# Kernel optimization log

Hardware: AMD Instinct MI355X
Metric: run time of the kernel (lower is better)

## Reference

```python
import jax, jax.numpy as jnp
import numpy as np

L, H = 6, 8          # n_layer, n_head
LN_EPS = 1e-5


def _ln(x, g, b):
    mu = jnp.mean(x, axis=-1, keepdims=True)
    var = jnp.mean((x - mu) ** 2, axis=-1, keepdims=True)
    return (x - mu) * jax.lax.rsqrt(var + LN_EPS) * g + b


def setup_inputs() -> dict:
    key = jax.random.key(0)
    B, T, V, D = 2, 2048, 32000, 512
    F = 4 * D
    std = 0.02
    ks = jax.random.split(key, 8)
    idx = jax.random.randint(ks[0], (B, T), 0, V)
    wte = jax.random.normal(ks[1], (V, D), dtype=jnp.float32) * std
    wpe = jax.random.normal(ks[2], (T, D), dtype=jnp.float32) * std
    qkv_w = jax.random.normal(ks[3], (L, D, 3 * D), dtype=jnp.float32) * std
    proj_w = jax.random.normal(ks[4], (L, D, D), dtype=jnp.float32) * std
    fc1_w = jax.random.normal(ks[5], (L, D, F), dtype=jnp.float32) * std
    fc2_w = jax.random.normal(ks[6], (L, F, D), dtype=jnp.float32) * std
    return dict(
        idx=idx, wte=wte, wpe=wpe,
        ln1_g=jnp.ones((L, D), jnp.float32), ln1_b=jnp.zeros((L, D), jnp.float32),
        qkv_w=qkv_w, qkv_b=jnp.zeros((L, 3 * D), jnp.float32),
        proj_w=proj_w, proj_b=jnp.zeros((L, D), jnp.float32),
        ln2_g=jnp.ones((L, D), jnp.float32), ln2_b=jnp.zeros((L, D), jnp.float32),
        fc1_w=fc1_w, fc1_b=jnp.zeros((L, F), jnp.float32),
        fc2_w=fc2_w, fc2_b=jnp.zeros((L, D), jnp.float32),
        lnf_g=jnp.ones((D,), jnp.float32), lnf_b=jnp.zeros((D,), jnp.float32),
    )


def reference(idx, wte, wpe, ln1_g, ln1_b, qkv_w, qkv_b, proj_w, proj_b,
              ln2_g, ln2_b, fc1_w, fc1_b, fc2_w, fc2_b, lnf_g, lnf_b):
    B, T = idx.shape
    D = wte.shape[1]
    hd = D // H
    scale = 1.0 / jnp.sqrt(jnp.asarray(hd, wte.dtype))
    x = wte[idx] + wpe[:T]                      # [B,T,D]
    mask = jnp.tril(jnp.ones((T, T), dtype=bool))

    def block(x, p):
        g1, b1, Wqkv, bqkv, Wp, bp, g2, b2, W1, bf1, W2, bf2 = p
        h = _ln(x, g1, b1)
        qkv = h @ Wqkv + bqkv                   # [B,T,3D]
        q, k, v = jnp.split(qkv, 3, axis=-1)
        q = q.reshape(B, T, H, hd)
        k = k.reshape(B, T, H, hd)
        v = v.reshape(B, T, H, hd)
        att = jnp.einsum('bqhd,bkhd->bhqk', q, k) * scale
        att = jnp.where(mask, att, -jnp.inf)
        att = jax.nn.softmax(att, axis=-1)
        y = jnp.einsum('bhqk,bkhd->bqhd', att, v).reshape(B, T, D)
        x = x + y @ Wp + bp
        h = _ln(x, g2, b2)
        x = x + jax.nn.gelu(h @ W1 + bf1, approximate=False) @ W2 + bf2
        return x, None

    x, _ = jax.lax.scan(block, x, (ln1_g, ln1_b, qkv_w, qkv_b, proj_w, proj_b,
                                   ln2_g, ln2_b, fc1_w, fc1_b, fc2_w, fc2_b))
    x = _ln(x, lnf_g, lnf_b)
    logits = x @ wte.T                          # tied head, [B,T,V]
    return logits
```

## Files before the change

kernel.cpp:

```cpp
#include <hip/hip_runtime.h>
#include <hip/hip_bf16.h>
#include <math.h>

#define BB 2
#define TT 2048
#define DD 512
#define HH 8
#define HD 64
#define FF 2048
#define VV 32000
#define LL 6
#define MM (BB * TT)

typedef unsigned int   u32;
typedef unsigned short u16;
typedef __attribute__((ext_vector_type(8))) short short8;
typedef __attribute__((ext_vector_type(4))) float f32x4;

__device__ __forceinline__ u16 f2bf_bits(float f)
{
    __hip_bfloat16 h = __float2bfloat16(f);
    u16 u;
    __builtin_memcpy(&u, &h, 2);
    return u;
}

__device__ __forceinline__ void gll16(const u16* g, u16* l)
{
    __builtin_amdgcn_global_load_lds(
        (const __attribute__((address_space(1))) u32*)g,
        (__attribute__((address_space(3))) u32*)l,
        16, 0, 0);
}

__device__ __forceinline__ float gelu_exact(float v)
{
    return 0.5f * v * (1.0f + erff(v * 0.70710678118654752440f));
}

__device__ __forceinline__ u16* swp(u16* base, int row, int col)
{
    int off = (row * 128 + col * 2) ^ ((row & 7) << 4);
    return (u16*)((char*)base + off);
}
__device__ __forceinline__ const u16* swpc(const u16* base, int row, int col)
{
    int off = (row * 128 + col * 2) ^ ((row & 7) << 4);
    return (const u16*)((const char*)base + off);
}

__global__ __launch_bounds__(128)
void embed_kernel(const int* __restrict__ idx, const float* __restrict__ wte,
                  const float* __restrict__ wpe, float* __restrict__ x)
{
    int row = blockIdx.x;
    int t = row & (TT - 1);
    int tok = idx[row];
    const float4* wt = (const float4*)(wte + (size_t)tok * DD);
    const float4* wp = (const float4*)(wpe + (size_t)t * DD);
    float4 a = wt[threadIdx.x];
    float4 p = wp[threadIdx.x];
    float4 r;
    r.x = a.x + p.x; r.y = a.y + p.y; r.z = a.z + p.z; r.w = a.w + p.w;
    ((float4*)(x + (size_t)row * DD))[threadIdx.x] = r;
}

__global__ __launch_bounds__(256)
void ln_kernel(const float* __restrict__ x, const float* __restrict__ g,
               const float* __restrict__ b, u16* __restrict__ out)
{
    int row = blockIdx.x;
    const float* xr = x + (size_t)row * DD;
    int tid = threadIdx.x;
    float v1 = xr[tid], v2 = xr[tid + 256];
    float s = v1 + v2;
    float ss = v1 * v1 + v2 * v2;
    #pragma unroll
    for (int o = 32; o; o >>= 1) {
        s  += __shfl_xor(s, o);
        ss += __shfl_xor(ss, o);
    }
    __shared__ float sred[4], ssred[4];
    int wid = tid >> 6, lane = tid & 63;
    if (lane == 0) { sred[wid] = s; ssred[wid] = ss; }
    __syncthreads();
    s  = sred[0] + sred[1] + sred[2] + sred[3];
    ss = ssred[0] + ssred[1] + ssred[2] + ssred[3];
    float mu  = s * (1.0f / DD);
    float var = ss * (1.0f / DD) - mu * mu;
    float rs  = rsqrtf(var + 1e-5f);
    u16* orow = out + (size_t)row * DD;
    orow[tid]       = f2bf_bits((v1 - mu) * rs * g[tid]       + b[tid]);
    orow[tid + 256] = f2bf_bits((v2 - mu) * rs * g[tid + 256] + b[tid + 256]);
}

__global__ __launch_bounds__(256)
void weight_prep_kernel(const float* __restrict__ qkv_w, const float* __restrict__ proj_w,
                        const float* __restrict__ fc1_w, const float* __restrict__ fc2_w,
                        u16* __restrict__ wqa, u16* __restrict__ wpa,
                        u16* __restrict__ w1a, u16* __restrict__ w2a)
{
    int id = blockIdx.x;
    int l = id / 3072, r = id % 3072;
    const float* in; u16* out; int K, N, tt;
    if (r < 768)       { in = qkv_w + (size_t)l * DD * 3 * DD; out = wqa + (size_t)l * 3 * DD * DD; K = DD; N = 3 * DD; tt = r; }
    else if (r < 1024) { in = proj_w + (size_t)l * DD * DD;    out = wpa + (size_t)l * DD * DD;    K = DD; N = DD;     tt = r - 768; }
    else if (r < 2048) { in = fc1_w + (size_t)l * DD * FF;     out = w1a + (size_t)l * DD * FF;    K = DD; N = FF;     tt = r - 1024; }
    else               { in = fc2_w + (size_t)l * FF * DD;     out = w2a + (size_t)l * FF * DD;    K = FF; N = DD;     tt = r - 2048; }
    int ntx = N >> 5;
    int n0 = (tt % ntx) << 5, k0 = (tt / ntx) << 5;
    __shared__ float tile[32][33];
    int tx = threadIdx.x & 31, ty = threadIdx.x >> 5;
    #pragma unroll
    for (int i = 0; i < 4; ++i)
        tile[ty + i * 8][tx] = in[(size_t)(k0 + ty + i * 8) * N + n0 + tx];
    __syncthreads();
    #pragma unroll
    for (int i = 0; i < 4; ++i)
        out[(size_t)(n0 + ty + i * 8) * K + k0 + tx] = f2bf_bits(tile[tx][ty + i * 8]);
}

__global__ __launch_bounds__(256)
void cvt_kernel(const float* __restrict__ in, u16* __restrict__ out, int n4)
{
    int i = blockIdx.x * 256 + threadIdx.x;
    if (i >= n4) return;
    float4 v = ((const float4*)in)[i];
    ushort4 o;
    o.x = f2bf_bits(v.x); o.y = f2bf_bits(v.y);
    o.z = f2bf_bits(v.z); o.w = f2bf_bits(v.w);
    ((ushort4*)out)[i] = o;
}

template<int BN, bool GELU_ACT, bool RESID, bool OUTBF16, bool QKV_SPLIT>
__global__ __launch_bounds__(256)
void mfma_gemm(const u16* __restrict__ A, const u16* __restrict__ Bt,
               const float* __restrict__ bias, const float* __restrict__ resid,
               void* __restrict__ Cout, u16* __restrict__ Vout,
               int M, int N, int K)
{
    constexpr int NJ = BN / 32;
    __shared__ u16 As[128 * 64];
    __shared__ u16 Bs[BN * 64];

    const int tid  = threadIdx.x;
    const int lane = tid & 63;
    const int w    = tid >> 6;
    const int wr   = w >> 1, wc = w & 1;

    const int nbx = gridDim.x;
    const int nwg = nbx * gridDim.y;
    int bid = blockIdx.y * nbx + blockIdx.x;
    int swz = (bid & 7) * (nwg >> 3) + (bid >> 3);
    const int m0 = (swz / nbx) * 128;
    const int n0 = (swz % nbx) * BN;

    const int trow = tid >> 3;
    const int tcol = (tid & 7) * 8;
    const u16* ga = A  + (size_t)(m0 + trow) * K + tcol;
    const u16* gb = Bt + (size_t)(n0 + trow) * K + tcol;
    u16* la = As + tid * 8;
    u16* lb = Bs + tid * 8;

    f32x4 acc[4][NJ] = {};

    const int fr = lane & 15;
    const int fk = (lane >> 4) * 8;

    for (int k0 = 0; k0 < K; k0 += 64) {
        #pragma unroll
        for (int p = 0; p < 4; ++p)
            gll16(ga + k0 + (size_t)p * 32 * K, la + p * 2048);
        #pragma unroll
        for (int p = 0; p < NJ; ++p)
            gll16(gb + k0 + (size_t)p * 32 * K, lb + p * 2048);
        asm volatile("s_waitcnt vmcnt(0)" ::: "memory");
        __syncthreads();

        #pragma unroll
        for (int ks = 0; ks < 2; ++ks) {
            short8 af[4], bfr[NJ];
            #pragma unroll
            for (int f = 0; f < 4; ++f)
                af[f]  = *(const short8*)&As[(wr * 64 + f * 16 + fr) * 64 + ks * 32 + fk];
            #pragma unroll
            for (int f = 0; f < NJ; ++f)
                bfr[f] = *(const short8*)&Bs[(wc * (BN / 2) + f * 16 + fr) * 64 + ks * 32 + fk];
            #pragma unroll
            for (int i = 0; i < 4; ++i)
                #pragma unroll
                for (int j = 0; j < NJ; ++j)
                    acc[i][j] = __builtin_amdgcn_mfma_f32_16x16x32_bf16(
                        af[i], bfr[j], acc[i][j], 0, 0, 0);
        }
        __syncthreads();
    }

    const int c0 = n0 + wc * (BN / 2) + fr;
    const int r0 = m0 + wr * 64 + ((lane >> 4) << 2);
    #pragma unroll
    for (int j = 0; j < NJ; ++j) {
        const int c = c0 + j * 16;
        const float bv = bias ? bias[c] : 0.0f;
        #pragma unroll
        for (int i = 0; i < 4; ++i) {
            #pragma unroll
            for (int r = 0; r < 4; ++r) {
                const int row = r0 + i * 16 + r;
                float v = acc[i][j][r] + bv;
                if constexpr (GELU_ACT) v = gelu_exact(v);
                if constexpr (RESID) v += resid[(size_t)row * N + c];
                if constexpr (QKV_SPLIT) {
                    if (c < 1024) {
                        ((u16*)Cout)[(size_t)row * 1024 + c] = f2bf_bits(v);
                    } else {
                        const int t = row & (TT - 1);
                        Vout[(((size_t)(row >> 11) * 512 + (c - 1024)) << 11) + t] = f2bf_bits(v);
                    }
                } else if constexpr (OUTBF16) {
                    ((u16*)Cout)[(size_t)row * N + c] = f2bf_bits(v);
                } else {
                    ((float*)Cout)[(size_t)row * N + c] = v;
                }
            }
        }
    }
}

__global__ __launch_bounds__(256)
void attn_kernel(const u16* __restrict__ qkb, const u16* __restrict__ vtb,
                 u16* __restrict__ y)
{
    const int l = blockIdx.x;
    const int u = l & 255, v = l >> 8;
    const int bh = u & 15;
    const int half = u >> 4;
    const int qt = v ? (16 + half) : (15 - half);
    const int h = bh & (HH - 1);
    const int b = bh >> 3;

    __shared__ alignas(16) u16 Qs[64 * 64];
    __shared__ alignas(16) u16 Ks[64 * 64];
    __shared__ alignas(16) u16 Vt[64 * 64];
    __shared__ alignas(16) u16 Ps[64 * 64];

    const int tid = threadIdx.x;
    const int lane = tid & 63;
    const int w = tid >> 6;
    const int ln = lane & 15, hi = lane >> 4;
    const int q0 = qt * 64;

    const u16* base  = qkb + (size_t)b * TT * 1024 + h * HD;
    const u16* vbase = vtb + (size_t)(b * 512 + h * HD) * TT;

    {
        int r = tid >> 2, c0 = (tid & 3) * 16;
        const u16* qrow = base + (size_t)(q0 + r) * 1024;
        *(short8*)swp(Qs, r, c0)     = *(const short8*)(qrow + c0);
        *(short8*)swp(Qs, r, c0 + 8) = *(const short8*)(qrow + c0 + 8);
    }

    float m[4], lsum[4];
    f32x4 oacc[4] = {};
    #pragma unroll
    for (int r = 0; r < 4; ++r) { m[r] = -INFINITY; lsum[r] = 0.0f; }

    for (int kt = 0; kt <= qt; ++kt) {
        const int k0 = kt * 64;
        __syncthreads();
        {
            int r = tid >> 2, c0 = (tid & 3) * 16;
            const u16* krow = base + (size_t)(k0 + r) * 1024 + 512;
            *(short8*)swp(Ks, r, c0)     = *(const short8*)(krow + c0);
            *(short8*)swp(Ks, r, c0 + 8) = *(const short8*)(krow + c0 + 8);
            const u16* vrow = vbase + (size_t)r * TT + k0;
            *(short8*)swp(Vt, r, c0)     = *(const short8*)(vrow + c0);
            *(short8*)swp(Vt, r, c0 + 8) = *(const short8*)(vrow + c0 + 8);
        }
        __syncthreads();

        short8 aq[2];
        #pragma unroll
        for (int ks = 0; ks < 2; ++ks)
            aq[ks] = *(const short8*)swpc(Qs, w * 16 + ln, ks * 32 + hi * 8);

        f32x4 sacc[4] = {};
        #pragma unroll
        for (int j = 0; j < 4; ++j)
            #pragma unroll
            for (int ks = 0; ks < 2; ++ks) {
                short8 bk = *(const short8*)swpc(Ks, j * 16 + ln, ks * 32 + hi * 8);
                sacc[j] = __builtin_amdgcn_mfma_f32_16x16x32_bf16(aq[ks], bk, sacc[j], 0, 0, 0);
            }

        const bool diag = (kt == qt);
        #pragma unroll
        for (int r = 0; r < 4; ++r) {
            const int qrow = w * 16 + hi * 4 + r;
            float sv[4];
            #pragma unroll
            for (int j = 0; j < 4; ++j) {
                float s = sacc[j][r] * 0.125f;
                if (diag && (j * 16 + ln > qrow)) s = -INFINITY;
                sv[j] = s;
            }
            float rm = fmaxf(fmaxf(sv[0], sv[1]), fmaxf(sv[2], sv[3]));
            #pragma unroll
            for (int o = 1; o < 16; o <<= 1) rm = fmaxf(rm, __shfl_xor(rm, o));
            float mn = fmaxf(m[r], rm);
            float corr = __expf(m[r] - mn);
            m[r] = mn;
            float ps = 0.0f;
            #pragma unroll
            for (int j = 0; j < 4; ++j) {
                float p = __expf(sv[j] - mn);
                ps += p;
                *swp(Ps, qrow, j * 16 + ln) = f2bf_bits(p);
            }
            #pragma unroll
            for (int o = 1; o < 16; o <<= 1) ps += __shfl_xor(ps, o);
            lsum[r] = lsum[r] * corr + ps;
            #pragma unroll
            for (int db = 0; db < 4; ++db) oacc[db][r] *= corr;
        }

        short8 ap[2];
        #pragma unroll
        for (int ks = 0; ks < 2; ++ks)
            ap[ks] = *(const short8*)swpc(Ps, w * 16 + ln, ks * 32 + hi * 8);
        #pragma unroll
        for (int db = 0; db < 4; ++db)
            #pragma unroll
            for (int ks = 0; ks < 2; ++ks) {
                short8 bv = *(const short8*)swpc(Vt, db * 16 + ln, ks * 32 + hi * 8);
                oacc[db] = __builtin_amdgcn_mfma_f32_16x16x32_bf16(ap[ks], bv, oacc[db], 0, 0, 0);
            }
    }

    #pragma unroll
    for (int r = 0; r < 4; ++r) {
        const int q = q0 + w * 16 + hi * 4 + r;
        const float inv = 1.0f / lsum[r];
        u16* yrow = y + (size_t)(b * TT + q) * DD + h * HD;
        #pragma unroll
        for (int db = 0; db < 4; ++db)
            yrow[db * 16 + ln] = f2bf_bits(oacc[db][r] * inv);
    }
}

extern "C" void kernel_launch(void* const* d_in, const int* in_sizes, int n_in,
                              void* d_out, int out_size, void* d_ws, size_t ws_size,
                              hipStream_t stream)
{
    const int*   idx    = (const int*)  d_in[0];
    const float* wte    = (const float*)d_in[1];
    const float* wpe    = (const float*)d_in[2];
    const float* ln1_g  = (const float*)d_in[3];
    const float* ln1_b  = (const float*)d_in[4];
    const float* qkv_w  = (const float*)d_in[5];
    const float* qkv_b  = (const float*)d_in[6];
    const float* proj_w = (const float*)d_in[7];
    const float* proj_b = (const float*)d_in[8];
    const float* ln2_g  = (const float*)d_in[9];
    const float* ln2_b  = (const float*)d_in[10];
    const float* fc1_w  = (const float*)d_in[11];
    const float* fc1_b  = (const float*)d_in[12];
    const float* fc2_w  = (const float*)d_in[13];
    const float* fc2_b  = (const float*)d_in[14];
    const float* lnf_g  = (const float*)d_in[15];
    const float* lnf_b  = (const float*)d_in[16];
    float* out = (float*)d_out;

    char* ws = (char*)d_ws;
    float* x    = (float*)(ws);
    u16*   h    = (u16*)(ws + ((size_t)8  << 20));
    u16*   y    = (u16*)(ws + ((size_t)12 << 20));
    u16*   qkb  = (u16*)(ws + ((size_t)16 << 20));
    u16*   vtb  = (u16*)(ws + ((size_t)24 << 20));
    u16*   wqa  = (u16*)(ws + ((size_t)28 << 20));
    u16*   wpa  = (u16*)(ws + ((size_t)38 << 20));
    u16*   w1a  = (u16*)(ws + ((size_t)42 << 20));
    u16*   w2a  = (u16*)(ws + ((size_t)55 << 20));
    u16*   ffb  = (u16*)(ws + ((size_t)68 << 20));
    u16*   wteb = (u16*)(ws + ((size_t)85 << 20));

    embed_kernel<<<MM, 128, 0, stream>>>(idx, wte, wpe, x);

    weight_prep_kernel<<<LL * 3072, 256, 0, stream>>>(
        qkv_w, proj_w, fc1_w, fc2_w, wqa, wpa, w1a, w2a);

    cvt_kernel<<<(VV * DD / 4 + 255) / 256, 256, 0, stream>>>(wte, wteb, VV * DD / 4);

    for (int l = 0; l < LL; ++l) {
        ln_kernel<<<MM, 256, 0, stream>>>(x, ln1_g + l * DD, ln1_b + l * DD, h);

        mfma_gemm<128, false, false, true, true><<<dim3(12, 32), 256, 0, stream>>>(
            h, wqa + (size_t)l * 3 * DD * DD, qkv_b + (size_t)l * 3 * DD,
            nullptr, qkb, vtb, MM, 3 * DD, DD);

        attn_kernel<<<512, 256, 0, stream>>>(qkb, vtb, y);

        mfma_gemm<64, false, true, false, false><<<dim3(8, 32), 256, 0, stream>>>(
            y, wpa + (size_t)l * DD * DD, proj_b + (size_t)l * DD,
            x, x, nullptr, MM, DD, DD);

        ln_kernel<<<MM, 256, 0, stream>>>(x, ln2_g + l * DD, ln2_b + l * DD, h);

        mfma_gemm<128, true, false, true, false><<<dim3(16, 32), 256, 0, stream>>>(
            h, w1a + (size_t)l * DD * FF, fc1_b + (size_t)l * FF,
            nullptr, ffb, nullptr, MM, FF, DD);

        mfma_gemm<64, false, true, false, false><<<dim3(8, 32), 256, 0, stream>>>(
            ffb, w2a + (size_t)l * FF * DD, fc2_b + (size_t)l * DD,
            x, x, nullptr, MM, DD, FF);
    }

    ln_kernel<<<MM, 256, 0, stream>>>(x, lnf_g, lnf_b, h);

    mfma_gemm<128, false, false, false, false><<<dim3(250, 32), 256, 0, stream>>>(
        h, wteb, nullptr, nullptr, out, nullptr, MM, VV, DD);
}
```

Baseline: 1.248 ms.

## Double-buffer K/V tiles with register prefetch in attention kernel

```diff
diff --git a/kernel.cpp b/kernel.cpp
--- a/kernel.cpp
+++ b/kernel.cpp
@@ -239,10 +239,10 @@
     const int h = bh & (HH - 1);
     const int b = bh >> 3;
 
-    __shared__ alignas(16) u16 Qs[64 * 64];
-    __shared__ alignas(16) u16 Ks[64 * 64];
-    __shared__ alignas(16) u16 Vt[64 * 64];
-    __shared__ alignas(16) u16 Ps[64 * 64];
+    __shared__ alignas(16) u16 Qs[4096];
+    __shared__ alignas(16) u16 Ks[2][4096];
+    __shared__ alignas(16) u16 Vt[2][4096];
+    __shared__ alignas(16) u16 Ps[4096];
 
     const int tid = threadIdx.x;
     const int lane = tid & 63;
@@ -253,11 +253,21 @@
     const u16* base  = qkb + (size_t)b * TT * 1024 + h * HD;
     const u16* vbase = vtb + (size_t)(b * 512 + h * HD) * TT;
 
+    const int sr = tid >> 2, sc = (tid & 3) * 16;
+
     {
-        int r = tid >> 2, c0 = (tid & 3) * 16;
-        const u16* qrow = base + (size_t)(q0 + r) * 1024;
-        *(short8*)swp(Qs, r, c0)     = *(const short8*)(qrow + c0);
-        *(short8*)swp(Qs, r, c0 + 8) = *(const short8*)(qrow + c0 + 8);
+        const u16* qrow = base + (size_t)(q0 + sr) * 1024;
+        *(short8*)swp(Qs, sr, sc)     = *(const short8*)(qrow + sc);
+        *(short8*)swp(Qs, sr, sc + 8) = *(const short8*)(qrow + sc + 8);
+    }
+    short8 rk0, rk1, rv0, rv1;
+    {
+        const u16* krow = base + (size_t)sr * 1024 + 512;
+        rk0 = *(const short8*)(krow + sc);
+        rk1 = *(const short8*)(krow + sc + 8);
+        const u16* vrow = vbase + (size_t)sr * TT;
+        rv0 = *(const short8*)(vrow + sc);
+        rv1 = *(const short8*)(vrow + sc + 8);
     }
 
     float m[4], lsum[4];
@@ -266,32 +276,40 @@
     for (int r = 0; r < 4; ++r) { m[r] = -INFINITY; lsum[r] = 0.0f; }
 
     for (int kt = 0; kt <= qt; ++kt) {
-        const int k0 = kt * 64;
+        u16* ks = Ks[kt & 1];
+        u16* vt = Vt[kt & 1];
+
+        *(short8*)swp(ks, sr, sc)     = rk0;
+        *(short8*)swp(ks, sr, sc + 8) = rk1;
+        *(short8*)swp(vt, sr, sc)     = rv0;
+        *(short8*)swp(vt, sr, sc + 8) = rv1;
         __syncthreads();
-        {
-            int r = tid >> 2, c0 = (tid & 3) * 16;
-            const u16* krow = base + (size_t)(k0 + r) * 1024 + 512;
-            *(short8*)swp(Ks, r, c0)     = *(const short8*)(krow + c0);
-            *(short8*)swp(Ks, r, c0 + 8) = *(const short8*)(krow + c0 + 8);
-            const u16* vrow = vbase + (size_t)r * TT + k0;
-            *(short8*)swp(Vt, r, c0)     = *(const short8*)(vrow + c0);
-            *(short8*)swp(Vt, r, c0 + 8) = *(const short8*)(vrow + c0 + 8);
+
+        if (kt < qt) {
+            const int k0n = (kt + 1) * 64;
+            const u16* krow = base + (size_t)(k0n + sr) * 1024 + 512;
+            rk0 = *(const short8*)(krow + sc);
+            rk1 = *(const short8*)(krow + sc + 8);
+            const u16* vrow = vbase + (size_t)sr * TT + k0n;
+            rv0 = *(const short8*)(vrow + sc);
+            rv1 = *(const short8*)(vrow + sc + 8);
         }
-        __syncthreads();
 
         short8 aq[2];
         #pragma unroll
-        for (int ks = 0; ks < 2; ++ks)
-            aq[ks] = *(const short8*)swpc(Qs, w * 16 + ln, ks * 32 + hi * 8);
+        for (int s2 = 0; s2 < 2; ++s2)
+            aq[s2] = *(const short8*)swpc(Qs, w * 16 + ln, s2 * 32 + hi * 8);
 
         f32x4 sacc[4] = {};
+        __builtin_amdgcn_s_setprio(1);
         #pragma unroll
         for (int j = 0; j < 4; ++j)
             #pragma unroll
-            for (int ks = 0; ks < 2; ++ks) {
-                short8 bk = *(const short8*)swpc(Ks, j * 16 + ln, ks * 32 + hi * 8);
-                sacc[j] = __builtin_amdgcn_mfma_f32_16x16x32_bf16(aq[ks], bk, sacc[j], 0, 0, 0);
+            for (int s2 = 0; s2 < 2; ++s2) {
+                short8 bk = *(const short8*)swpc(ks, j * 16 + ln, s2 * 32 + hi * 8);
+                sacc[j] = __builtin_amdgcn_mfma_f32_16x16x32_bf16(aq[s2], bk, sacc[j], 0, 0, 0);
             }
+        __builtin_amdgcn_s_setprio(0);
 
         const bool diag = (kt == qt);
         #pragma unroll
@@ -326,15 +344,17 @@
 
         short8 ap[2];
         #pragma unroll
-        for (int ks = 0; ks < 2; ++ks)
-            ap[ks] = *(const short8*)swpc(Ps, w * 16 + ln, ks * 32 + hi * 8);
+        for (int s2 = 0; s2 < 2; ++s2)
+            ap[s2] = *(const short8*)swpc(Ps, w * 16 + ln, s2 * 32 + hi * 8);
+        __builtin_amdgcn_s_setprio(1);
         #pragma unroll
         for (int db = 0; db < 4; ++db)
             #pragma unroll
-            for (int ks = 0; ks < 2; ++ks) {
-                short8 bv = *(const short8*)swpc(Vt, db * 16 + ln, ks * 32 + hi * 8);
-                oacc[db] = __builtin_amdgcn_mfma_f32_16x16x32_bf16(ap[ks], bv, oacc[db], 0, 0, 0);
+            for (int s2 = 0; s2 < 2; ++s2) {
+                short8 bv = *(const short8*)swpc(vt, db * 16 + ln, s2 * 32 + hi * 8);
+                oacc[db] = __builtin_amdgcn_mfma_f32_16x16x32_bf16(ap[s2], bv, oacc[db], 0, 0, 0);
             }
+        __builtin_amdgcn_s_setprio(0);
     }
 
     #pragma unroll
```

Result: faster. 1.195 ms (-4.2%).
